# Kernel tuning notes

Measured on AMD Instinct MI355X. Metric: run time of the kernel, lower is better.

The kernel has to match this reference:

```python
import jax, jax.numpy as jnp
import numpy as np

S = 192          # seq_len = h*w = 24*8
FF = 2048        # dim_feedforward
CH = [171, 171, 170]  # d_model=512 chunked over 3 layers
EPS = 1e-5


def _bn(x, axes):
    # training-mode BatchNorm with gamma=1, beta=0 (default init; xavier only touches dim>1 weights)
    m = x.mean(axis=axes, keepdims=True)
    v = x.var(axis=axes, keepdims=True)
    return (x - m) / jnp.sqrt(v + EPS)


def _layer(tgt, mem, fc1_w, fc1_b, se, fc2_w, fc2_b, fc3_w, fc3_b):
    # tgt: [q, s, d], mem: [k, s, d]
    q, s, d = tgt.shape
    k = mem.shape[0]
    qy = tgt @ fc1_w.T + fc1_b            # [q, s, d]
    ky = mem @ fc1_w.T + fc1_b            # [k, s, d]
    # correlation volume gated by learned sigmoid bias -> [q, k, s, t]
    vol = jnp.einsum('qtd,ksd->qkst', qy, ky) * jax.nn.sigmoid(se)
    sc = jnp.concatenate([vol.max(axis=2).reshape(q * k, s),   # max over s -> per-t
                          vol.max(axis=3).reshape(q * k, s)],  # max over t -> per-s
                         axis=-1)                               # [q*k, 2s]
    sc = _bn(sc.reshape(-1, 1, s), (0, 2)).reshape(-1, s)       # bn1 over (N, L)
    sc = jax.nn.relu(_bn(sc @ fc2_w.T + fc2_b, (0,)))           # fc2 + bn2 + relu
    sc = sc @ fc3_w.T + fc3_b                                   # [2*q*k, 1]
    sc = _bn(sc.reshape(-1, 2).sum(-1, keepdims=True), (0,))    # combine halves + bn3
    return sc.reshape(q, k)


def _forward(gallery, query, params):
    # gallery/query: NCHW -> [B, H, W, C]; tgt = gallery (memory in TransMatcher), memory arg = query
    g = jnp.transpose(gallery, (0, 2, 3, 1))
    f = jnp.transpose(query, (0, 2, 3, 1))
    q, k = g.shape[0], f.shape[0]
    g = g.reshape(q, S, -1)
    f = f.reshape(k, S, -1)
    start = 0
    score = jnp.zeros((q, k), dtype=g.dtype)
    for i, c in enumerate(CH):
        score = score + _layer(g[..., start:start + c], f[..., start:start + c], *params[i])
        start += c
    # decoder norm: BatchNorm1d(1) over flattened scores
    return _bn(score.reshape(-1, 1), (0,)).reshape(q, k)


def setup_inputs() -> dict:
    key = jax.random.key(0)
    ks = iter(jax.random.split(key, 32))
    d = {
        'gallery': jax.random.normal(next(ks), (32, 512, 24, 8), jnp.float32),
        'query': jax.random.normal(next(ks), (32, 512, 24, 8), jnp.float32),
    }
    def xavier(k, shape):
        fan_in, fan_out = shape[1], shape[0]
        lim = np.sqrt(6.0 / (fan_in + fan_out)).astype(np.float32)
        return jax.random.uniform(k, shape, jnp.float32, -lim, lim)
    for i, c in enumerate(CH):
        d[f'l{i}_fc1_w'] = xavier(next(ks), (c, c))
        d[f'l{i}_fc1_b'] = jax.random.normal(next(ks), (c,), jnp.float32) * 0.02
        d[f'l{i}_se'] = xavier(next(ks), (S, S))
        d[f'l{i}_fc2_w'] = xavier(next(ks), (FF, S))
        d[f'l{i}_fc2_b'] = jax.random.normal(next(ks), (FF,), jnp.float32) * 0.02
        d[f'l{i}_fc3_w'] = xavier(next(ks), (1, FF))
        d[f'l{i}_fc3_b'] = jax.random.normal(next(ks), (1,), jnp.float32) * 0.02
    return d


def reference(gallery, query,
              l0_fc1_w, l0_fc1_b, l0_se, l0_fc2_w, l0_fc2_b, l0_fc3_w, l0_fc3_b,
              l1_fc1_w, l1_fc1_b, l1_se, l1_fc2_w, l1_fc2_b, l1_fc3_w, l1_fc3_b,
              l2_fc1_w, l2_fc1_b, l2_se, l2_fc2_w, l2_fc2_b, l2_fc3_w, l2_fc3_b):
    params = [
        (l0_fc1_w, l0_fc1_b, l0_se, l0_fc2_w, l0_fc2_b, l0_fc3_w, l0_fc3_b),
        (l1_fc1_w, l1_fc1_b, l1_se, l1_fc2_w, l1_fc2_b, l1_fc3_w, l1_fc3_b),
        (l2_fc1_w, l2_fc1_b, l2_se, l2_fc2_w, l2_fc2_b, l2_fc3_w, l2_fc3_b),
    ]
    return _forward(gallery, query, params)
```

## Files before the change

### kernel.cpp

```cpp
#include <hip/hip_runtime.h>
#include <math.h>

#define EPS 1e-5f
#define TOTAL_IN (32*512*192)
#define CPAD 176
#define KSTEPS 11
#define PACK_BK 6144

#define OFF_SIGSE 0u
#define OFF_W1T   110592u
#define OFF_QPACK 141568u
#define OFF_KPACK 1222912u
#define OFF_SC    2304256u
#define OFF_OUT2  2697472u
#define OFF_QSLAB OFF_OUT2
#define OFF_KSLAB (OFF_OUT2 + 1081344u)
#define OFF_COLP  6891776u
#define OFF_M2V2  7022848u
#define OFF_Y     7026944u
#define OFF_SCORE 7028992u

#define B_SIGSE 0u
#define B_W1T   110592u
#define B_SC    203520u
#define B_COLP  1383168u
#define B_M2R2  1579776u
#define B_Y     1592064u
#define B_SC3   1598208u
#define B_BIG   1601280u
#define B_SLAB  B_BIG
#define B_PACKF (B_BIG + 6488064u)
#define B_OUT2  B_BIG
#define B_TOTAL 14577408u

typedef __attribute__((ext_vector_type(8)))  short short8;
typedef __attribute__((ext_vector_type(16))) float f32x16;

__device__ __forceinline__ unsigned short f2bf(float x) {
    unsigned u = __float_as_uint(x);
    u += 0x7fffu + ((u >> 16) & 1u);
    return (unsigned short)(u >> 16);
}
__device__ __forceinline__ float bf2f(unsigned short h) {
    return __uint_as_float(((unsigned)h) << 16);
}

__device__ __forceinline__ void g2lds16(const void* g, void* l) {
    __builtin_amdgcn_global_load_lds((const __attribute__((address_space(1))) unsigned int*)g,
                                     (__attribute__((address_space(3))) unsigned int*)l, 16, 0, 0);
}

__global__ void k_sigse(const float* __restrict__ se0, const float* __restrict__ se1,
                        const float* __restrict__ se2, float* __restrict__ dst) {
    int idx = blockIdx.x * 256 + threadIdx.x;
    if (idx >= 3 * 36864) return;
    int l = idx / 36864, r = idx % 36864;
    const float* se = (l == 0) ? se0 : ((l == 1) ? se1 : se2);
    float x = se[r];
    dst[idx] = 1.0f / (1.0f + __expf(-x));
}


__global__ void k_w1t_b(const float* __restrict__ w1_0, const float* __restrict__ w1_1,
                        const float* __restrict__ w1_2, float* __restrict__ w1t) {
    int idx = blockIdx.x * 256 + threadIdx.x;
    if (idx >= 3 * CPAD * CPAD) return;
    int l = idx / (CPAD * CPAD), r = idx % (CPAD * CPAD);
    int i = r / CPAD, j = r % CPAD;
    int c = (l == 2) ? 170 : 171;
    const float* w1 = (l == 0) ? w1_0 : ((l == 1) ? w1_1 : w1_2);
    w1t[idx] = (i < c && j < c) ? w1[j * c + i] : 0.0f;
}

__global__ __launch_bounds__(256, 4)
void k_fc1_b(const float* __restrict__ g0, const float* __restrict__ g1,
             const float* __restrict__ w1tb,
             const float* __restrict__ b1_0, const float* __restrict__ b1_1,
             const float* __restrict__ b1_2, float* __restrict__ slabs) {
    __shared__ float As[2 * 16 * CPAD];
    __shared__ float Bs[2 * 16 * 64];
    const int quad = blockIdx.x, b = blockIdx.y, z = blockIdx.z;
    const int l = z >> 1, tensor = z & 1;
    const int c = (l == 2) ? 170 : 171, st = l * 171;
    const float* inp = tensor ? g1 : g0;
    const float* w1t = w1tb + (unsigned)l * (CPAD * CPAD);
    const float* b1 = (l == 0) ? b1_0 : ((l == 1) ? b1_1 : b1_2);
    float* dst = slabs + (size_t)z * 1081344u;
    const int tid = threadIdx.x, ty = tid >> 4, tx = tid & 15;
    const size_t boff = (size_t)b * 98304 + (size_t)st * 192 + (size_t)quad * 64;

    float acc[11][4];
#pragma unroll
    for (int i = 0; i < 11; ++i)
#pragma unroll
        for (int j = 0; j < 4; ++j) acc[i][j] = 0.0f;

    float4 v[4];
    auto load_chunk = [&](int ci) {
#pragma unroll
        for (int e = 0; e < 4; ++e) {
            int f = tid + (e << 8);
            if (f < 704) {
                v[e] = *(const float4*)(w1t + ci * 2816 + f * 4);
            } else if (f < 960) {
                int f2 = f - 704;
                int r = f2 >> 4, c4 = f2 & 15;
                size_t off = boff + (size_t)(ci * 16 + r) * 192 + c4 * 4;
                if (off > (size_t)(TOTAL_IN - 4)) off = (size_t)(TOTAL_IN - 4);
                v[e] = *(const float4*)(inp + off);
            }
        }
    };
    auto write_chunk = [&](int buf) {
        float* Ad = As + buf * 2816;
        float* Bd = Bs + buf * 1024;
#pragma unroll
        for (int e = 0; e < 4; ++e) {
            int f = tid + (e << 8);
            if (f < 704)      *(float4*)(Ad + f * 4) = v[e];
            else if (f < 960) *(float4*)(Bd + (f - 704) * 4) = v[e];
        }
    };

    load_chunk(0); write_chunk(0);
    __syncthreads();

    for (int ci = 0; ci < 11; ++ci) {
        const int buf = ci & 1;
        const bool pf = (ci + 1 < 11);
        if (pf) load_chunk(ci + 1);

        const float* Aw = As + buf * 2816 + ty * 11;
        const float* Bw = Bs + buf * 1024 + tx * 4;
#pragma unroll 2
        for (int kk = 0; kk < 16; ++kk) {
            float a[11];
#pragma unroll
            for (int i = 0; i < 11; ++i) a[i] = Aw[kk * CPAD + i];
            float4 B0 = *(const float4*)(Bw + kk * 64);
            float bb[4] = {B0.x, B0.y, B0.z, B0.w};
#pragma unroll
            for (int i = 0; i < 11; ++i)
#pragma unroll
                for (int j = 0; j < 4; ++j)
                    acc[i][j] = fmaf(a[i], bb[j], acc[i][j]);
        }
        if (pf) write_chunk(buf ^ 1);
        __syncthreads();
    }

    float* drow = dst + (size_t)b * (CPAD * 192) + quad * 64;
#pragma unroll
    for (int i = 0; i < 11; ++i) {
        int j = ty * 11 + i;
        bool valid = (j < c);
        float bias = valid ? b1[j] : 0.0f;
        float o[4];
#pragma unroll
        for (int jj = 0; jj < 4; ++jj) o[jj] = valid ? (acc[i][jj] + bias) : 0.0f;
        *(float4*)(drow + (size_t)j * 192 + tx * 4) = make_float4(o[0], o[1], o[2], o[3]);
    }
}

__global__ void k_pack_b(const float* __restrict__ slabs, short* __restrict__ packs) {
    const int kstep = blockIdx.x, b = blockIdx.y, z = blockIdx.z;
    const float* src = slabs + (size_t)z * 1081344u + (size_t)b * (CPAD * 192);
    short* dst = packs + (size_t)z * 2162688u + (size_t)(b * KSTEPS + kstep) * PACK_BK;
    const int t = threadIdx.x;
    const int tile = t >> 6, lane = t & 63;
    const int hf = (lane >> 5) & 1, col = lane & 31;
    const int dbase = kstep * 16 + hf * 8;
    const int x = tile * 32 + col;

    short8 H, L;
#pragma unroll
    for (int e = 0; e < 8; ++e) {
        float v = src[(size_t)(dbase + e) * 192 + x];
        unsigned short h = f2bf(v);
        unsigned short l = f2bf(v - bf2f(h));
        H[e] = (short)h;
        L[e] = (short)l;
    }
    ((short8*)dst)[(0 * 6 + tile) * 64 + lane] = H;
    ((short8*)dst)[(1 * 6 + tile) * 64 + lane] = L;
}

__global__ __launch_bounds__(256, 2)
void k_corr_b(const short* __restrict__ packs, const float* __restrict__ sigb,
              float* __restrict__ scb) {
    __shared__ short smem[2 * 12288];
    const int qk = blockIdx.x, l = blockIdx.y;
    const int q = qk >> 5, k = qk & 31;
    const int tid = threadIdx.x, lane = tid & 63, w = tid >> 6;
    const int ws = w >> 1, wt = w & 1;
    const short* qpack = packs + (size_t)(l * 2 + 0) * 2162688u;
    const short* kpack = packs + (size_t)(l * 2 + 1) * 2162688u;
    const float* sig = sigb + (unsigned)l * 36864u;
    float* sc = scb + (size_t)l * 393216u;
    const char* Abase = (const char*)(kpack + (size_t)k * KSTEPS * PACK_BK);
    const char* Bbase = (const char*)(qpack + (size_t)q * KSTEPS * PACK_BK);

    f32x16 acc[3][3];
#pragma unroll
    for (int i = 0; i < 3; ++i)
#pragma unroll
        for (int j = 0; j < 3; ++j)
#pragma unroll
            for (int r = 0; r < 16; ++r) acc[i][j][r] = 0.0f;

    auto stage = [&](int buf, int ks) {
#pragma unroll
        for (int u = 0; u < 6; ++u) {
            int c = u * 4 + w;
            const char* g = (c < 12 ? Abase + (size_t)ks * 12288 + c * 1024
                                    : Bbase + (size_t)ks * 12288 + (c - 12) * 1024) + lane * 16;
            g2lds16(g, (char*)smem + buf * 24576 + c * 1024);
        }
    };

    stage(0, 0);
    __syncthreads();

    int buf = 0;
    for (int ks = 0; ks < KSTEPS; ++ks) {
        if (ks + 1 < KSTEPS) stage(buf ^ 1, ks + 1);

        const short8* LA = (const short8*)((const char*)smem + buf * 24576);
        const short8* LB = (const short8*)((const char*)smem + buf * 24576 + 12288);
        short8 Ah[3], Al[3], Bh[3], Bl[3];
#pragma unroll
        for (int u = 0; u < 3; ++u) {
            Ah[u] = LA[(0 * 6 + ws * 3 + u) * 64 + lane];
            Al[u] = LA[(1 * 6 + ws * 3 + u) * 64 + lane];
            Bh[u] = LB[(0 * 6 + wt * 3 + u) * 64 + lane];
            Bl[u] = LB[(1 * 6 + wt * 3 + u) * 64 + lane];
        }
#pragma unroll
        for (int i = 0; i < 3; ++i)
#pragma unroll
            for (int j = 0; j < 3; ++j) {
                acc[i][j] = __builtin_amdgcn_mfma_f32_32x32x16_bf16(Ah[i], Bh[j], acc[i][j], 0, 0, 0);
                acc[i][j] = __builtin_amdgcn_mfma_f32_32x32x16_bf16(Al[i], Bh[j], acc[i][j], 0, 0, 0);
                acc[i][j] = __builtin_amdgcn_mfma_f32_32x32x16_bf16(Ah[i], Bl[j], acc[i][j], 0, 0, 0);
            }
        __syncthreads();
        buf ^= 1;
    }

    const int col = lane & 31, hf = lane >> 5;
    float* scr = (float*)smem;
    float cm[3] = {-3.0e38f, -3.0e38f, -3.0e38f};
#pragma unroll
    for (int i = 0; i < 3; ++i) {
        const int sbase = (ws * 3 + i) * 32;
        float rv[16];
#pragma unroll
        for (int r = 0; r < 16; ++r) rv[r] = -3.0e38f;
#pragma unroll
        for (int j = 0; j < 3; ++j) {
            const int tb = (wt * 3 + j) * 32 + col;
#pragma unroll
            for (int r = 0; r < 16; ++r) {
                int row = (r & 3) + 8 * (r >> 2) + 4 * hf;
                float v = acc[i][j][r] * sig[(size_t)(sbase + row) * 192 + tb];
                rv[r] = fmaxf(rv[r], v);
                cm[j] = fmaxf(cm[j], v);
            }
        }
#pragma unroll
        for (int m = 1; m < 32; m <<= 1)
#pragma unroll
            for (int r = 0; r < 16; ++r) rv[r] = fmaxf(rv[r], __shfl_xor(rv[r], m));
#pragma unroll
        for (int r = 0; r < 16; ++r)
            if (col == r)
                scr[384 + wt * 192 + sbase + (r & 3) + 8 * (r >> 2) + 4 * hf] = rv[r];
    }
#pragma unroll
    for (int j = 0; j < 3; ++j) {
        float c2 = fmaxf(cm[j], __shfl_xor(cm[j], 32));
        if (hf == 0) scr[ws * 192 + (wt * 3 + j) * 32 + col] = c2;
    }
    __syncthreads();
    if (tid < 192) {
        sc[(size_t)(2 * qk) * 192 + tid]     = fmaxf(scr[tid], scr[192 + tid]);
        sc[(size_t)(2 * qk + 1) * 192 + tid] = fmaxf(scr[384 + tid], scr[384 + 192 + tid]);
    }
}

__global__ __launch_bounds__(256, 2)
void k_fc2c_b(const float* __restrict__ scb,
              const float* __restrict__ w2_0, const float* __restrict__ w2_1,
              const float* __restrict__ w2_2,
              float* __restrict__ out2b, float* __restrict__ colpb) {
    __shared__ float Ast[32 * 132];
    __shared__ float Bst[32 * 132];
    const int bm = blockIdx.x & 15, bn = blockIdx.x >> 4, l = blockIdx.y;
    const float* sc = scb + (size_t)l * 393216u;
    const float* w2 = (l == 0) ? w2_0 : ((l == 1) ? w2_1 : w2_2);
    float* out2 = out2b + (size_t)l * 4194304u;
    float* colp = colpb + (size_t)l * 65536u;
    const int r0 = bm * 128, c0 = bn * 128;
    const int tid = threadIdx.x, ty = tid >> 4, tx = tid & 15;
    const int r = tid >> 1, half = (tid & 1) * 16;

    float acc[8][8];
#pragma unroll
    for (int i = 0; i < 8; ++i)
#pragma unroll
        for (int j = 0; j < 8; ++j) acc[i][j] = 0.0f;

    for (int t0 = 0; t0 < 192; t0 += 32) {
        float4 av[4], bv[4];
        const float4* ga = (const float4*)(sc + (size_t)(r0 + r) * 192 + t0 + half);
        const float4* gb = (const float4*)(w2 + (size_t)(c0 + r) * 192 + t0 + half);
#pragma unroll
        for (int e = 0; e < 4; ++e) { av[e] = ga[e]; bv[e] = gb[e]; }
        __syncthreads();
#pragma unroll
        for (int e = 0; e < 4; ++e) {
            int t = half + 4 * e;
            Ast[(t + 0) * 132 + r] = av[e].x;  Bst[(t + 0) * 132 + r] = bv[e].x;
            Ast[(t + 1) * 132 + r] = av[e].y;  Bst[(t + 1) * 132 + r] = bv[e].y;
            Ast[(t + 2) * 132 + r] = av[e].z;  Bst[(t + 2) * 132 + r] = bv[e].z;
            Ast[(t + 3) * 132 + r] = av[e].w;  Bst[(t + 3) * 132 + r] = bv[e].w;
        }
        __syncthreads();
#pragma unroll 4
        for (int kk = 0; kk < 32; ++kk) {
            const float4* ap = (const float4*)(Ast + kk * 132 + ty * 8);
            const float4* bp = (const float4*)(Bst + kk * 132 + tx * 8);
            float4 A0 = ap[0], A1 = ap[1];
            float4 B0 = bp[0], B1 = bp[1];
            float a[8] = {A0.x, A0.y, A0.z, A0.w, A1.x, A1.y, A1.z, A1.w};
            float b[8] = {B0.x, B0.y, B0.z, B0.w, B1.x, B1.y, B1.z, B1.w};
#pragma unroll
            for (int i = 0; i < 8; ++i)
#pragma unroll
                for (int j = 0; j < 8; ++j)
                    acc[i][j] = fmaf(a[i], b[j], acc[i][j]);
        }
    }
#pragma unroll
    for (int i = 0; i < 8; ++i) {
        float4* op = (float4*)(out2 + (size_t)(r0 + ty * 8 + i) * 2048 + c0 + tx * 8);
        op[0] = make_float4(acc[i][0], acc[i][1], acc[i][2], acc[i][3]);
        op[1] = make_float4(acc[i][4], acc[i][5], acc[i][6], acc[i][7]);
    }
    float cs_[8], cq_[8];
#pragma unroll
    for (int jj = 0; jj < 8; ++jj) {
        float s = 0.0f, q2 = 0.0f;
#pragma unroll
        for (int i = 0; i < 8; ++i) { float v = acc[i][jj]; s += v; q2 += v * v; }
        cs_[jj] = s; cq_[jj] = q2;
    }
    __syncthreads();
#pragma unroll
    for (int jj = 0; jj < 8; ++jj) {
        Ast[ty * 128 + tx * 8 + jj] = cs_[jj];
        Bst[ty * 128 + tx * 8 + jj] = cq_[jj];
    }
    __syncthreads();
    if (tid < 128) {
        float s = 0.0f, q2 = 0.0f;
#pragma unroll
        for (int wv = 0; wv < 16; ++wv) { s += Ast[wv * 128 + tid]; q2 += Bst[wv * 128 + tid]; }
        colp[((size_t)bm * 2048 + c0 + tid) * 2 + 0] = s;
        colp[((size_t)bm * 2048 + c0 + tid) * 2 + 1] = q2;
    }
}

__global__ void k_colf_b(const float* __restrict__ colpb, float* __restrict__ m2r2b) {
    const int idx = blockIdx.x * 256 + threadIdx.x;
    if (idx >= 3 * 2048) return;
    const int l = idx >> 11, j = idx & 2047;
    const float* colp = colpb + (size_t)l * 65536u;
    float s = 0.0f, s2 = 0.0f;
    for (int bm = 0; bm < 16; ++bm) {
        s  += colp[((size_t)bm * 2048 + j) * 2 + 0];
        s2 += colp[((size_t)bm * 2048 + j) * 2 + 1];
    }
    float m = s * (1.0f / 2048.0f);
    float var = s2 * (1.0f / 2048.0f) - m * m;
    m2r2b[(size_t)l * 4096 + j * 2 + 0] = m;
    m2r2b[(size_t)l * 4096 + j * 2 + 1] = rsqrtf(var + EPS);
}

__global__ void k_fc3_b(const float* __restrict__ out2b, const float* __restrict__ m2r2b,
                        const float* __restrict__ w3_0, const float* __restrict__ w3_1,
                        const float* __restrict__ w3_2, float* __restrict__ yb) {
    const int rr = blockIdx.x, l = blockIdx.y;
    const float* out2 = out2b + (size_t)l * 4194304u;
    const float* m2r2 = m2r2b + (size_t)l * 4096u;
    const float* w3 = (l == 0) ? w3_0 : ((l == 1) ? w3_1 : w3_2);
    const int tid = threadIdx.x;
    __shared__ float red[4];
    float s = 0.0f;
    for (int j = tid; j < 2048; j += 256) {
        float2 mr = ((const float2*)m2r2)[j];
        float vv = (out2[(size_t)rr * 2048 + j] - mr.x) * mr.y;
        vv = fmaxf(vv, 0.0f);
        s += vv * w3[j];
    }
#pragma unroll
    for (int off = 32; off; off >>= 1) s += __shfl_xor(s, off);
    if ((tid & 63) == 0) red[tid >> 6] = s;
    __syncthreads();
    if (tid == 0) yb[(size_t)l * 2048 + rr] = red[0] + red[1] + red[2] + red[3];
}

__global__ void k_bn3_b(const float* __restrict__ yb, float* __restrict__ sc3) {
    const int l = blockIdx.x, tid = threadIdx.x;
    const float* y = yb + (size_t)l * 2048u;
    __shared__ float rs[4], rs2[4];
    float p[4]; float s = 0.0f, s2 = 0.0f;
#pragma unroll
    for (int u = 0; u < 4; ++u) {
        int i = tid + (u << 8);
        float vv = y[2 * i] + y[2 * i + 1];
        p[u] = vv; s += vv; s2 += vv * vv;
    }
#pragma unroll
    for (int off = 32; off; off >>= 1) { s += __shfl_xor(s, off); s2 += __shfl_xor(s2, off); }
    if ((tid & 63) == 0) { rs[tid >> 6] = s; rs2[tid >> 6] = s2; }
    __syncthreads();
    float S = rs[0] + rs[1] + rs[2] + rs[3];
    float S2 = rs2[0] + rs2[1] + rs2[2] + rs2[3];
    float m = S * (1.0f / 1024.0f);
    float var = S2 * (1.0f / 1024.0f) - m * m;
    float rstd = rsqrtf(var + EPS);
#pragma unroll
    for (int u = 0; u < 4; ++u) {
        int i = tid + (u << 8);
        sc3[(size_t)l * 1024 + i] = (p[u] - m) * rstd;
    }
}

__global__ void k_final3(const float* __restrict__ sc3, float* __restrict__ out) {
    const int tid = threadIdx.x;
    __shared__ float rs[4], rs2[4];
    float p[4]; float s = 0.0f, s2 = 0.0f;
#pragma unroll
    for (int u = 0; u < 4; ++u) {
        int i = tid + (u << 8);
        float vv = sc3[i] + sc3[1024 + i] + sc3[2048 + i];
        p[u] = vv; s += vv; s2 += vv * vv;
    }
#pragma unroll
    for (int off = 32; off; off >>= 1) { s += __shfl_xor(s, off); s2 += __shfl_xor(s2, off); }
    if ((tid & 63) == 0) { rs[tid >> 6] = s; rs2[tid >> 6] = s2; }
    __syncthreads();
    float S = rs[0] + rs[1] + rs[2] + rs[3];
    float S2 = rs2[0] + rs2[1] + rs2[2] + rs2[3];
    float m = S * (1.0f / 1024.0f);
    float var = S2 * (1.0f / 1024.0f) - m * m;
    float rstd = rsqrtf(var + EPS);
#pragma unroll
    for (int u = 0; u < 4; ++u) {
        int i = tid + (u << 8);
        out[i] = (p[u] - m) * rstd;
    }
}


__global__ void k_w1t(const float* __restrict__ w1, int c, float* __restrict__ w1t) {
    int idx = blockIdx.x * 256 + threadIdx.x;
    if (idx >= CPAD * CPAD) return;
    int i = idx / CPAD, j = idx % CPAD;
    w1t[idx] = (i < c && j < c) ? w1[j * c + i] : 0.0f;
}

__global__ __launch_bounds__(256, 4)
void k_fc1(const float* __restrict__ g0, const float* __restrict__ g1,
           const float* __restrict__ w1t, const float* __restrict__ b1,
           int c, int st, float* __restrict__ d0, float* __restrict__ d1) {
    __shared__ float As[2 * 16 * CPAD];
    __shared__ float Bs[2 * 16 * 64];
    const int quad = blockIdx.x, b = blockIdx.y, tensor = blockIdx.z;
    const float* inp = tensor ? g1 : g0;
    float* dst = tensor ? d1 : d0;
    const int tid = threadIdx.x, ty = tid >> 4, tx = tid & 15;
    const size_t boff = (size_t)b * 98304 + (size_t)st * 192 + (size_t)quad * 64;

    float acc[11][4];
#pragma unroll
    for (int i = 0; i < 11; ++i)
#pragma unroll
        for (int j = 0; j < 4; ++j) acc[i][j] = 0.0f;

    float4 v[4];
    auto load_chunk = [&](int ci) {
#pragma unroll
        for (int e = 0; e < 4; ++e) {
            int f = tid + (e << 8);
            if (f < 704) {
                v[e] = *(const float4*)(w1t + ci * 2816 + f * 4);
            } else if (f < 960) {
                int f2 = f - 704;
                int r = f2 >> 4, c4 = f2 & 15;
                size_t off = boff + (size_t)(ci * 16 + r) * 192 + c4 * 4;
                if (off > (size_t)(TOTAL_IN - 4)) off = (size_t)(TOTAL_IN - 4);
                v[e] = *(const float4*)(inp + off);
            }
        }
    };
    auto write_chunk = [&](int buf) {
        float* Ad = As + buf * 2816;
        float* Bd = Bs + buf * 1024;
#pragma unroll
        for (int e = 0; e < 4; ++e) {
            int f = tid + (e << 8);
            if (f < 704)      *(float4*)(Ad + f * 4) = v[e];
            else if (f < 960) *(float4*)(Bd + (f - 704) * 4) = v[e];
        }
    };

    load_chunk(0); write_chunk(0);
    __syncthreads();

    for (int ci = 0; ci < 11; ++ci) {
        const int buf = ci & 1;
        const bool pf = (ci + 1 < 11);
        if (pf) load_chunk(ci + 1);

        const float* Aw = As + buf * 2816 + ty * 11;
        const float* Bw = Bs + buf * 1024 + tx * 4;
#pragma unroll 2
        for (int kk = 0; kk < 16; ++kk) {
            float a[11];
#pragma unroll
            for (int i = 0; i < 11; ++i) a[i] = Aw[kk * CPAD + i];
            float4 B0 = *(const float4*)(Bw + kk * 64);
            float bb[4] = {B0.x, B0.y, B0.z, B0.w};
#pragma unroll
            for (int i = 0; i < 11; ++i)
#pragma unroll
                for (int j = 0; j < 4; ++j)
                    acc[i][j] = fmaf(a[i], bb[j], acc[i][j]);
        }
        if (pf) write_chunk(buf ^ 1);
        __syncthreads();
    }

    float* drow = dst + (size_t)b * (CPAD * 192) + quad * 64;
#pragma unroll
    for (int i = 0; i < 11; ++i) {
        int j = ty * 11 + i;
        bool valid = (j < c);
        float bias = valid ? b1[j] : 0.0f;
        float o[4];
#pragma unroll
        for (int jj = 0; jj < 4; ++jj) o[jj] = valid ? (acc[i][jj] + bias) : 0.0f;
        *(float4*)(drow + (size_t)j * 192 + tx * 4) = make_float4(o[0], o[1], o[2], o[3]);
    }
}

__global__ void k_pack(const float* __restrict__ qslab, const float* __restrict__ kslab,
                       short* __restrict__ qpack, short* __restrict__ kpack) {
    const int kstep = blockIdx.x, b = blockIdx.y, tensor = blockIdx.z;
    const float* src = (tensor ? kslab : qslab) + (size_t)b * (CPAD * 192);
    short* dst = (tensor ? kpack : qpack) + (size_t)(b * KSTEPS + kstep) * PACK_BK;
    const int t = threadIdx.x;
    const int tile = t >> 6, lane = t & 63;
    const int hf = (lane >> 5) & 1, col = lane & 31;
    const int dbase = kstep * 16 + hf * 8;
    const int x = tile * 32 + col;

    short8 H, L;
#pragma unroll
    for (int e = 0; e < 8; ++e) {
        float v = src[(size_t)(dbase + e) * 192 + x];
        unsigned short h = f2bf(v);
        unsigned short l = f2bf(v - bf2f(h));
        H[e] = (short)h;
        L[e] = (short)l;
    }
    ((short8*)dst)[(0 * 6 + tile) * 64 + lane] = H;
    ((short8*)dst)[(1 * 6 + tile) * 64 + lane] = L;
}

__global__ __launch_bounds__(256, 2)
void k_corr(const short* __restrict__ qpack, const short* __restrict__ kpack,
            const float* __restrict__ sig, float* __restrict__ sc) {
    __shared__ short smem[2 * 12288];
    const int qk = blockIdx.x, q = qk >> 5, k = qk & 31;
    const int tid = threadIdx.x, lane = tid & 63, w = tid >> 6;
    const int ws = w >> 1, wt = w & 1;
    const char* Abase = (const char*)(kpack + (size_t)k * KSTEPS * PACK_BK);
    const char* Bbase = (const char*)(qpack + (size_t)q * KSTEPS * PACK_BK);

    f32x16 acc[3][3];
#pragma unroll
    for (int i = 0; i < 3; ++i)
#pragma unroll
        for (int j = 0; j < 3; ++j)
#pragma unroll
            for (int r = 0; r < 16; ++r) acc[i][j][r] = 0.0f;

    auto stage = [&](int buf, int ks) {
#pragma unroll
        for (int u = 0; u < 6; ++u) {
            int c = u * 4 + w;
            const char* g = (c < 12 ? Abase + (size_t)ks * 12288 + c * 1024
                                    : Bbase + (size_t)ks * 12288 + (c - 12) * 1024) + lane * 16;
            g2lds16(g, (char*)smem + buf * 24576 + c * 1024);
        }
    };

    stage(0, 0);
    __syncthreads();

    int buf = 0;
    for (int ks = 0; ks < KSTEPS; ++ks) {
        if (ks + 1 < KSTEPS) stage(buf ^ 1, ks + 1);

        const short8* LA = (const short8*)((const char*)smem + buf * 24576);
        const short8* LB = (const short8*)((const char*)smem + buf * 24576 + 12288);
        short8 Ah[3], Al[3], Bh[3], Bl[3];
#pragma unroll
        for (int u = 0; u < 3; ++u) {
            Ah[u] = LA[(0 * 6 + ws * 3 + u) * 64 + lane];
            Al[u] = LA[(1 * 6 + ws * 3 + u) * 64 + lane];
            Bh[u] = LB[(0 * 6 + wt * 3 + u) * 64 + lane];
            Bl[u] = LB[(1 * 6 + wt * 3 + u) * 64 + lane];
        }
#pragma unroll
        for (int i = 0; i < 3; ++i)
#pragma unroll
            for (int j = 0; j < 3; ++j) {
                acc[i][j] = __builtin_amdgcn_mfma_f32_32x32x16_bf16(Ah[i], Bh[j], acc[i][j], 0, 0, 0);
                acc[i][j] = __builtin_amdgcn_mfma_f32_32x32x16_bf16(Al[i], Bh[j], acc[i][j], 0, 0, 0);
                acc[i][j] = __builtin_amdgcn_mfma_f32_32x32x16_bf16(Ah[i], Bl[j], acc[i][j], 0, 0, 0);
            }
        __syncthreads();
        buf ^= 1;
    }

    const int col = lane & 31, hf = lane >> 5;
    float* scr = (float*)smem;
    float cm[3] = {-3.0e38f, -3.0e38f, -3.0e38f};
#pragma unroll
    for (int i = 0; i < 3; ++i) {
        const int sbase = (ws * 3 + i) * 32;
        float rv[16];
#pragma unroll
        for (int r = 0; r < 16; ++r) rv[r] = -3.0e38f;
#pragma unroll
        for (int j = 0; j < 3; ++j) {
            const int tb = (wt * 3 + j) * 32 + col;
#pragma unroll
            for (int r = 0; r < 16; ++r) {
                int row = (r & 3) + 8 * (r >> 2) + 4 * hf;
                float v = acc[i][j][r] * sig[(size_t)(sbase + row) * 192 + tb];
                rv[r] = fmaxf(rv[r], v);
                cm[j] = fmaxf(cm[j], v);
            }
        }
#pragma unroll
        for (int m = 1; m < 32; m <<= 1)
#pragma unroll
            for (int r = 0; r < 16; ++r) rv[r] = fmaxf(rv[r], __shfl_xor(rv[r], m));
#pragma unroll
        for (int r = 0; r < 16; ++r)
            if (col == r)
                scr[384 + wt * 192 + sbase + (r & 3) + 8 * (r >> 2) + 4 * hf] = rv[r];
    }
#pragma unroll
    for (int j = 0; j < 3; ++j) {
        float c2 = fmaxf(cm[j], __shfl_xor(cm[j], 32));
        if (hf == 0) scr[ws * 192 + (wt * 3 + j) * 32 + col] = c2;
    }
    __syncthreads();
    if (tid < 192) {
        sc[(size_t)(2 * qk) * 192 + tid]     = fmaxf(scr[tid], scr[192 + tid]);
        sc[(size_t)(2 * qk + 1) * 192 + tid] = fmaxf(scr[384 + tid], scr[384 + 192 + tid]);
    }
}

__global__ __launch_bounds__(256, 2)
void k_fc2(const float* __restrict__ sc, const float* __restrict__ w2, float* __restrict__ out2) {
    __shared__ float Ast[32 * 132];
    __shared__ float Bst[32 * 132];
    const int bm = blockIdx.x & 15, bn = blockIdx.x >> 4;
    const int r0 = bm * 128, c0 = bn * 128;
    const int tid = threadIdx.x, ty = tid >> 4, tx = tid & 15;
    const int r = tid >> 1, half = (tid & 1) * 16;

    float acc[8][8];
#pragma unroll
    for (int i = 0; i < 8; ++i)
#pragma unroll
        for (int j = 0; j < 8; ++j) acc[i][j] = 0.0f;

    for (int t0 = 0; t0 < 192; t0 += 32) {
        float4 av[4], bv[4];
        const float4* ga = (const float4*)(sc + (size_t)(r0 + r) * 192 + t0 + half);
        const float4* gb = (const float4*)(w2 + (size_t)(c0 + r) * 192 + t0 + half);
#pragma unroll
        for (int e = 0; e < 4; ++e) { av[e] = ga[e]; bv[e] = gb[e]; }
        __syncthreads();
#pragma unroll
        for (int e = 0; e < 4; ++e) {
            int t = half + 4 * e;
            Ast[(t + 0) * 132 + r] = av[e].x;  Bst[(t + 0) * 132 + r] = bv[e].x;
            Ast[(t + 1) * 132 + r] = av[e].y;  Bst[(t + 1) * 132 + r] = bv[e].y;
            Ast[(t + 2) * 132 + r] = av[e].z;  Bst[(t + 2) * 132 + r] = bv[e].z;
            Ast[(t + 3) * 132 + r] = av[e].w;  Bst[(t + 3) * 132 + r] = bv[e].w;
        }
        __syncthreads();
#pragma unroll 4
        for (int kk = 0; kk < 32; ++kk) {
            const float4* ap = (const float4*)(Ast + kk * 132 + ty * 8);
            const float4* bp = (const float4*)(Bst + kk * 132 + tx * 8);
            float4 A0 = ap[0], A1 = ap[1];
            float4 B0 = bp[0], B1 = bp[1];
            float a[8] = {A0.x, A0.y, A0.z, A0.w, A1.x, A1.y, A1.z, A1.w};
            float b[8] = {B0.x, B0.y, B0.z, B0.w, B1.x, B1.y, B1.z, B1.w};
#pragma unroll
            for (int i = 0; i < 8; ++i)
#pragma unroll
                for (int j = 0; j < 8; ++j)
                    acc[i][j] = fmaf(a[i], b[j], acc[i][j]);
        }
    }
#pragma unroll
    for (int i = 0; i < 8; ++i) {
        float4* op = (float4*)(out2 + (size_t)(r0 + ty * 8 + i) * 2048 + c0 + tx * 8);
        op[0] = make_float4(acc[i][0], acc[i][1], acc[i][2], acc[i][3]);
        op[1] = make_float4(acc[i][4], acc[i][5], acc[i][6], acc[i][7]);
    }
}

__global__ void k_colp(const float* __restrict__ out2, float* __restrict__ colp) {
    const int bc = blockIdx.x & 7, br = blockIdx.x >> 3;
    const int j = bc * 256 + threadIdx.x;
    float s = 0.0f, s2 = 0.0f;
    for (int rr = br * 64; rr < br * 64 + 64; ++rr) {
        float vv = out2[(size_t)rr * 2048 + j];
        s += vv; s2 += vv * vv;
    }
    colp[((size_t)br * 2048 + j) * 2 + 0] = s;
    colp[((size_t)br * 2048 + j) * 2 + 1] = s2;
}

__global__ void k_colf(const float* __restrict__ colp, float* __restrict__ m2r2) {
    const int j = blockIdx.x * 256 + threadIdx.x;
    if (j >= 2048) return;
    float s = 0.0f, s2 = 0.0f;
    for (int br = 0; br < 32; ++br) {
        s  += colp[((size_t)br * 2048 + j) * 2 + 0];
        s2 += colp[((size_t)br * 2048 + j) * 2 + 1];
    }
    float m = s * (1.0f / 2048.0f);
    float var = s2 * (1.0f / 2048.0f) - m * m;
    m2r2[j * 2 + 0] = m;
    m2r2[j * 2 + 1] = rsqrtf(var + EPS);
}

__global__ void k_fc3(const float* __restrict__ out2, const float* __restrict__ m2r2,
                      const float* __restrict__ w3, float* __restrict__ y) {
    const int rr = blockIdx.x;
    const int tid = threadIdx.x;
    __shared__ float red[4];
    float s = 0.0f;
    for (int j = tid; j < 2048; j += 256) {
        float2 mr = ((const float2*)m2r2)[j];
        float vv = (out2[(size_t)rr * 2048 + j] - mr.x) * mr.y;
        vv = fmaxf(vv, 0.0f);
        s += vv * w3[j];
    }
#pragma unroll
    for (int off = 32; off; off >>= 1) s += __shfl_xor(s, off);
    if ((tid & 63) == 0) red[tid >> 6] = s;
    __syncthreads();
    if (tid == 0) y[rr] = red[0] + red[1] + red[2] + red[3];
}

__global__ void k_bn3(const float* __restrict__ y, float* __restrict__ score, int first) {
    const int tid = threadIdx.x;
    __shared__ float rs[4], rs2[4];
    float p[4]; float s = 0.0f, s2 = 0.0f;
#pragma unroll
    for (int u = 0; u < 4; ++u) {
        int i = tid + (u << 8);
        float vv = y[2 * i] + y[2 * i + 1];
        p[u] = vv; s += vv; s2 += vv * vv;
    }
#pragma unroll
    for (int off = 32; off; off >>= 1) { s += __shfl_xor(s, off); s2 += __shfl_xor(s2, off); }
    if ((tid & 63) == 0) { rs[tid >> 6] = s; rs2[tid >> 6] = s2; }
    __syncthreads();
    float S = rs[0] + rs[1] + rs[2] + rs[3];
    float S2 = rs2[0] + rs2[1] + rs2[2] + rs2[3];
    float m = S * (1.0f / 1024.0f);
    float var = S2 * (1.0f / 1024.0f) - m * m;
    float rstd = rsqrtf(var + EPS);
#pragma unroll
    for (int u = 0; u < 4; ++u) {
        int i = tid + (u << 8);
        float vv = (p[u] - m) * rstd;
        score[i] = first ? vv : (score[i] + vv);
    }
}

__global__ void k_final(const float* __restrict__ score, float* __restrict__ out) {
    const int tid = threadIdx.x;
    __shared__ float rs[4], rs2[4];
    float p[4]; float s = 0.0f, s2 = 0.0f;
#pragma unroll
    for (int u = 0; u < 4; ++u) {
        int i = tid + (u << 8);
        float vv = score[i];
        p[u] = vv; s += vv; s2 += vv * vv;
    }
#pragma unroll
    for (int off = 32; off; off >>= 1) { s += __shfl_xor(s, off); s2 += __shfl_xor(s2, off); }
    if ((tid & 63) == 0) { rs[tid >> 6] = s; rs2[tid >> 6] = s2; }
    __syncthreads();
    float S = rs[0] + rs[1] + rs[2] + rs[3];
    float S2 = rs2[0] + rs2[1] + rs2[2] + rs2[3];
    float m = S * (1.0f / 1024.0f);
    float var = S2 * (1.0f / 1024.0f) - m * m;
    float rstd = rsqrtf(var + EPS);
#pragma unroll
    for (int u = 0; u < 4; ++u) {
        int i = tid + (u << 8);
        out[i] = (p[u] - m) * rstd;
    }
}

extern "C" void kernel_launch(void* const* d_in, const int* in_sizes, int n_in,
                              void* d_out, int out_size, void* d_ws, size_t ws_size,
                              hipStream_t stream) {
    const float* gallery = (const float*)d_in[0];
    const float* query   = (const float*)d_in[1];
    float* ws = (float*)d_ws;

    const bool batched = (ws_size >= (size_t)B_TOTAL * sizeof(float));

    if (batched) {
        k_sigse<<<(3 * 36864 + 255) / 256, 256, 0, stream>>>(
            (const float*)d_in[2 + 0 * 7 + 2], (const float*)d_in[2 + 1 * 7 + 2],
            (const float*)d_in[2 + 2 * 7 + 2], ws + B_SIGSE);
        k_w1t_b<<<(3 * CPAD * CPAD + 255) / 256, 256, 0, stream>>>(
            (const float*)d_in[2 + 0 * 7 + 0], (const float*)d_in[2 + 1 * 7 + 0],
            (const float*)d_in[2 + 2 * 7 + 0], ws + B_W1T);
        k_fc1_b<<<dim3(3, 32, 6), 256, 0, stream>>>(
            gallery, query, ws + B_W1T,
            (const float*)d_in[2 + 0 * 7 + 1], (const float*)d_in[2 + 1 * 7 + 1],
            (const float*)d_in[2 + 2 * 7 + 1], ws + B_SLAB);
        k_pack_b<<<dim3(KSTEPS, 32, 6), 384, 0, stream>>>(ws + B_SLAB, (short*)(ws + B_PACKF));
        k_corr_b<<<dim3(1024, 3), 256, 0, stream>>>((const short*)(ws + B_PACKF),
                                                    ws + B_SIGSE, ws + B_SC);
        k_fc2c_b<<<dim3(256, 3), 256, 0, stream>>>(
            ws + B_SC,
            (const float*)d_in[2 + 0 * 7 + 3], (const float*)d_in[2 + 1 * 7 + 3],
            (const float*)d_in[2 + 2 * 7 + 3], ws + B_OUT2, ws + B_COLP);
        k_colf_b<<<24, 256, 0, stream>>>(ws + B_COLP, ws + B_M2R2);
        k_fc3_b<<<dim3(2048, 3), 256, 0, stream>>>(
            ws + B_OUT2, ws + B_M2R2,
            (const float*)d_in[2 + 0 * 7 + 5], (const float*)d_in[2 + 1 * 7 + 5],
            (const float*)d_in[2 + 2 * 7 + 5], ws + B_Y);
        k_bn3_b<<<3, 256, 0, stream>>>(ws + B_Y, ws + B_SC3);
        k_final3<<<1, 256, 0, stream>>>(ws + B_SC3, (float*)d_out);
        return;
    }

    const int cs[3] = {171, 171, 170};
    const int st[3] = {0, 171, 342};

    short* qpack = (short*)(ws + OFF_QPACK);
    short* kpack = (short*)(ws + OFF_KPACK);

    k_sigse<<<(3 * 36864 + 255) / 256, 256, 0, stream>>>(
        (const float*)d_in[2 + 0 * 7 + 2], (const float*)d_in[2 + 1 * 7 + 2],
        (const float*)d_in[2 + 2 * 7 + 2], ws + OFF_SIGSE);

    for (int l = 0; l < 3; ++l) {
        const float* w1 = (const float*)d_in[2 + l * 7 + 0];
        const float* b1 = (const float*)d_in[2 + l * 7 + 1];
        const float* w2 = (const float*)d_in[2 + l * 7 + 3];
        const float* w3 = (const float*)d_in[2 + l * 7 + 5];

        k_w1t<<<(CPAD * CPAD + 255) / 256, 256, 0, stream>>>(w1, cs[l], ws + OFF_W1T);
        k_fc1<<<dim3(3, 32, 2), 256, 0, stream>>>(gallery, query, ws + OFF_W1T, b1,
                                                  cs[l], st[l], ws + OFF_QSLAB, ws + OFF_KSLAB);
        k_pack<<<dim3(KSTEPS, 32, 2), 384, 0, stream>>>(ws + OFF_QSLAB, ws + OFF_KSLAB,
                                                        qpack, kpack);
        k_corr<<<1024, 256, 0, stream>>>(qpack, kpack, ws + OFF_SIGSE + l * 36864, ws + OFF_SC);
        k_fc2<<<256, 256, 0, stream>>>(ws + OFF_SC, w2, ws + OFF_OUT2);
        k_colp<<<256, 256, 0, stream>>>(ws + OFF_OUT2, ws + OFF_COLP);
        k_colf<<<8, 256, 0, stream>>>(ws + OFF_COLP, ws + OFF_M2V2);
        k_fc3<<<2048, 256, 0, stream>>>(ws + OFF_OUT2, ws + OFF_M2V2, w3, ws + OFF_Y);
        k_bn3<<<1, 256, 0, stream>>>(ws + OFF_Y, ws + OFF_SCORE, l == 0 ? 1 : 0);
    }
    k_final<<<1, 256, 0, stream>>>(ws + OFF_SCORE, (float*)d_out);
}
```

Before: 389.0 us.

## Move fc2 GEMM onto bf16x3 MFMA with packed operands from corr kernel

Replaces the FP32 SIMT fc2 GEMM with a split-bf16 (hi/lo, three-product) MFMA kernel. The corr kernel now writes its pooled scores directly in the MFMA-packed hi/lo bf16 layout, and a new kernel pre-packs fc2 weights the same way. The fc1 kernel also pads its weight tile to 12 rows per thread so it can use float4 LDS loads. This targets the FP32 FMA cost of the 2048x2048x192 GEMMs, at the price of an extra packing launch, a larger workspace, and a small precision change from the bf16x3 approximation.

Measured after the change: 373.2 us. -4.1%, faster.

```diff
diff --git a/kernel.cpp b/kernel.cpp
--- a/kernel.cpp
+++ b/kernel.cpp
@@ -4,6 +4,7 @@
 #define EPS 1e-5f
 #define TOTAL_IN (32*512*192)
 #define CPAD 176
+#define MPAD 192
 #define KSTEPS 11
 #define PACK_BK 6144
 
@@ -22,16 +23,17 @@
 
 #define B_SIGSE 0u
 #define B_W1T   110592u
-#define B_SC    203520u
-#define B_COLP  1383168u
-#define B_M2R2  1579776u
-#define B_Y     1592064u
-#define B_SC3   1598208u
-#define B_BIG   1601280u
+#define B_SCPF  211968u
+#define B_W2PF  1391616u
+#define B_COLP  2571264u
+#define B_M2R2  2767872u
+#define B_Y     2780160u
+#define B_SC3   2786304u
+#define B_BIG   2789376u
 #define B_SLAB  B_BIG
 #define B_PACKF (B_BIG + 6488064u)
 #define B_OUT2  B_BIG
-#define B_TOTAL 14577408u
+#define B_TOTAL 15765504u
 
 typedef __attribute__((ext_vector_type(8)))  short short8;
 typedef __attribute__((ext_vector_type(16))) float f32x16;
@@ -64,9 +66,9 @@
 __global__ void k_w1t_b(const float* __restrict__ w1_0, const float* __restrict__ w1_1,
                         const float* __restrict__ w1_2, float* __restrict__ w1t) {
     int idx = blockIdx.x * 256 + threadIdx.x;
-    if (idx >= 3 * CPAD * CPAD) return;
-    int l = idx / (CPAD * CPAD), r = idx % (CPAD * CPAD);
-    int i = r / CPAD, j = r % CPAD;
+    if (idx >= 3 * CPAD * MPAD) return;
+    int l = idx / (CPAD * MPAD), r = idx % (CPAD * MPAD);
+    int i = r / MPAD, j = r % MPAD;
     int c = (l == 2) ? 170 : 171;
     const float* w1 = (l == 0) ? w1_0 : ((l == 1) ? w1_1 : w1_2);
     w1t[idx] = (i < c && j < c) ? w1[j * c + i] : 0.0f;
@@ -77,21 +79,21 @@
              const float* __restrict__ w1tb,
              const float* __restrict__ b1_0, const float* __restrict__ b1_1,
              const float* __restrict__ b1_2, float* __restrict__ slabs) {
-    __shared__ float As[2 * 16 * CPAD];
+    __shared__ float As[2 * 16 * MPAD];
     __shared__ float Bs[2 * 16 * 64];
     const int quad = blockIdx.x, b = blockIdx.y, z = blockIdx.z;
     const int l = z >> 1, tensor = z & 1;
     const int c = (l == 2) ? 170 : 171, st = l * 171;
     const float* inp = tensor ? g1 : g0;
-    const float* w1t = w1tb + (unsigned)l * (CPAD * CPAD);
+    const float* w1t = w1tb + (unsigned)l * (CPAD * MPAD);
     const float* b1 = (l == 0) ? b1_0 : ((l == 1) ? b1_1 : b1_2);
     float* dst = slabs + (size_t)z * 1081344u;
     const int tid = threadIdx.x, ty = tid >> 4, tx = tid & 15;
     const size_t boff = (size_t)b * 98304 + (size_t)st * 192 + (size_t)quad * 64;
 
-    float acc[11][4];
-#pragma unroll
-    for (int i = 0; i < 11; ++i)
+    float acc[12][4];
+#pragma unroll
+    for (int i = 0; i < 12; ++i)
 #pragma unroll
         for (int j = 0; j < 4; ++j) acc[i][j] = 0.0f;
 
@@ -100,10 +102,10 @@
 #pragma unroll
         for (int e = 0; e < 4; ++e) {
             int f = tid + (e << 8);
-            if (f < 704) {
-                v[e] = *(const float4*)(w1t + ci * 2816 + f * 4);
-            } else if (f < 960) {
-                int f2 = f - 704;
+            if (f < 768) {
+                v[e] = *(const float4*)(w1t + ci * 3072 + f * 4);
+            } else {
+                int f2 = f - 768;
                 int r = f2 >> 4, c4 = f2 & 15;
                 size_t off = boff + (size_t)(ci * 16 + r) * 192 + c4 * 4;
                 if (off > (size_t)(TOTAL_IN - 4)) off = (size_t)(TOTAL_IN - 4);
@@ -112,13 +114,13 @@
         }
     };
     auto write_chunk = [&](int buf) {
-        float* Ad = As + buf * 2816;
+        float* Ad = As + buf * 3072;
         float* Bd = Bs + buf * 1024;
 #pragma unroll
         for (int e = 0; e < 4; ++e) {
             int f = tid + (e << 8);
-            if (f < 704)      *(float4*)(Ad + f * 4) = v[e];
-            else if (f < 960) *(float4*)(Bd + (f - 704) * 4) = v[e];
+            if (f < 768) *(float4*)(Ad + f * 4) = v[e];
+            else         *(float4*)(Bd + (f - 768) * 4) = v[e];
         }
     };
 
@@ -130,17 +132,17 @@
         const bool pf = (ci + 1 < 11);
         if (pf) load_chunk(ci + 1);
 
-        const float* Aw = As + buf * 2816 + ty * 11;
+        const float* Aw = As + buf * 3072 + ty * 12;
         const float* Bw = Bs + buf * 1024 + tx * 4;
 #pragma unroll 2
         for (int kk = 0; kk < 16; ++kk) {
-            float a[11];
-#pragma unroll
-            for (int i = 0; i < 11; ++i) a[i] = Aw[kk * CPAD + i];
+            const float4* ap = (const float4*)(Aw + kk * MPAD);
+            float4 A0 = ap[0], A1 = ap[1], A2 = ap[2];
+            float a[12] = {A0.x, A0.y, A0.z, A0.w, A1.x, A1.y, A1.z, A1.w, A2.x, A2.y, A2.z, A2.w};
             float4 B0 = *(const float4*)(Bw + kk * 64);
             float bb[4] = {B0.x, B0.y, B0.z, B0.w};
 #pragma unroll
-            for (int i = 0; i < 11; ++i)
+            for (int i = 0; i < 12; ++i)
 #pragma unroll
                 for (int j = 0; j < 4; ++j)
                     acc[i][j] = fmaf(a[i], bb[j], acc[i][j]);
@@ -151,8 +153,9 @@
 
     float* drow = dst + (size_t)b * (CPAD * 192) + quad * 64;
 #pragma unroll
-    for (int i = 0; i < 11; ++i) {
-        int j = ty * 11 + i;
+    for (int i = 0; i < 12; ++i) {
+        int j = ty * 12 + i;
+        if (j >= CPAD) continue;
         bool valid = (j < c);
         float bias = valid ? b1[j] : 0.0f;
         float o[4];
@@ -185,9 +188,34 @@
     ((short8*)dst)[(1 * 6 + tile) * 64 + lane] = L;
 }
 
+__global__ void k_w2p(const float* __restrict__ w2_0, const float* __restrict__ w2_1,
+                      const float* __restrict__ w2_2, short* __restrict__ w2p) {
+    const int jt = blockIdx.x, l = blockIdx.y;
+    const float* w2 = (l == 0) ? w2_0 : ((l == 1) ? w2_1 : w2_2);
+    short* WP = w2p + (size_t)l * 786432u;
+    const int tid = threadIdx.x, lane = tid & 63, sub = tid >> 6;
+    const int j = jt * 32 + (lane & 31), hf = lane >> 5;
+#pragma unroll
+    for (int kk = 0; kk < 3; ++kk) {
+        int ks = sub * 3 + kk;
+        const float4* src = (const float4*)(w2 + (size_t)j * 192 + ks * 16 + hf * 8);
+        float4 a = src[0], b = src[1];
+        float v[8] = {a.x, a.y, a.z, a.w, b.x, b.y, b.z, b.w};
+        short8 H, L;
+#pragma unroll
+        for (int e = 0; e < 8; ++e) {
+            unsigned short h = f2bf(v[e]);
+            H[e] = (short)h;
+            L[e] = (short)f2bf(v[e] - bf2f(h));
+        }
+        ((short8*)WP)[((jt * 12 + ks) * 2 + 0) * 64 + lane] = H;
+        ((short8*)WP)[((jt * 12 + ks) * 2 + 1) * 64 + lane] = L;
+    }
+}
+
 __global__ __launch_bounds__(256, 2)
 void k_corr_b(const short* __restrict__ packs, const float* __restrict__ sigb,
-              float* __restrict__ scb) {
+              short* __restrict__ scp) {
     __shared__ short smem[2 * 12288];
     const int qk = blockIdx.x, l = blockIdx.y;
     const int q = qk >> 5, k = qk & 31;
@@ -196,7 +224,7 @@
     const short* qpack = packs + (size_t)(l * 2 + 0) * 2162688u;
     const short* kpack = packs + (size_t)(l * 2 + 1) * 2162688u;
     const float* sig = sigb + (unsigned)l * 36864u;
-    float* sc = scb + (size_t)l * 393216u;
+    short* scpl = scp + (size_t)l * 786432u;
     const char* Abase = (const char*)(kpack + (size_t)k * KSTEPS * PACK_BK);
     const char* Bbase = (const char*)(qpack + (size_t)q * KSTEPS * PACK_BK);
 
@@ -282,92 +310,116 @@
         if (hf == 0) scr[ws * 192 + (wt * 3 + j) * 32 + col] = c2;
     }
     __syncthreads();
-    if (tid < 192) {
-        sc[(size_t)(2 * qk) * 192 + tid]     = fmaxf(scr[tid], scr[192 + tid]);
-        sc[(size_t)(2 * qk + 1) * 192 + tid] = fmaxf(scr[384 + tid], scr[384 + 192 + tid]);
+    if (tid < 96) {
+        const int row = tid / 48, rem = tid % 48;
+        const int ks2 = rem >> 2, hf2 = (rem >> 1) & 1, pl = rem & 1;
+        const int r = 2 * qk + row;
+        const float* s0 = scr + row * 384;
+        short8 o;
+#pragma unroll
+        for (int e = 0; e < 8; ++e) {
+            int t = ks2 * 16 + hf2 * 8 + e;
+            float v = fmaxf(s0[t], s0[192 + t]);
+            unsigned short h = f2bf(v);
+            o[e] = pl ? (short)f2bf(v - bf2f(h)) : (short)h;
+        }
+        ((short8*)scpl)[(((r >> 5) * 12 + ks2) * 2 + pl) * 64 + (hf2 * 32 + (r & 31))] = o;
     }
 }
 
 __global__ __launch_bounds__(256, 2)
-void k_fc2c_b(const float* __restrict__ scb,
-              const float* __restrict__ w2_0, const float* __restrict__ w2_1,
-              const float* __restrict__ w2_2,
+void k_fc2m_b(const short* __restrict__ scp, const short* __restrict__ w2p,
               float* __restrict__ out2b, float* __restrict__ colpb) {
-    __shared__ float Ast[32 * 132];
-    __shared__ float Bst[32 * 132];
-    const int bm = blockIdx.x & 15, bn = blockIdx.x >> 4, l = blockIdx.y;
-    const float* sc = scb + (size_t)l * 393216u;
-    const float* w2 = (l == 0) ? w2_0 : ((l == 1) ? w2_1 : w2_2);
+    __shared__ short smem[2 * 8192];
+    const int rblk = blockIdx.x & 15, nblk = blockIdx.x >> 4, l = blockIdx.y;
     float* out2 = out2b + (size_t)l * 4194304u;
     float* colp = colpb + (size_t)l * 65536u;
-    const int r0 = bm * 128, c0 = bn * 128;
-    const int tid = threadIdx.x, ty = tid >> 4, tx = tid & 15;
-    const int r = tid >> 1, half = (tid & 1) * 16;
-
-    float acc[8][8];
-#pragma unroll
-    for (int i = 0; i < 8; ++i)
-#pragma unroll
-        for (int j = 0; j < 8; ++j) acc[i][j] = 0.0f;
-
-    for (int t0 = 0; t0 < 192; t0 += 32) {
-        float4 av[4], bv[4];
-        const float4* ga = (const float4*)(sc + (size_t)(r0 + r) * 192 + t0 + half);
-        const float4* gb = (const float4*)(w2 + (size_t)(c0 + r) * 192 + t0 + half);
-#pragma unroll
-        for (int e = 0; e < 4; ++e) { av[e] = ga[e]; bv[e] = gb[e]; }
+    const int tid = threadIdx.x, lane = tid & 63, w = tid >> 6;
+    const int wr = w >> 1, wc = w & 1;
+    const char* SPb = (const char*)(scp + (size_t)l * 786432u + (size_t)rblk * 4 * 12288u);
+    const char* WPb = (const char*)(w2p + (size_t)l * 786432u + (size_t)nblk * 4 * 12288u);
+
+    f32x16 acc[2][2];
+#pragma unroll
+    for (int i = 0; i < 2; ++i)
+#pragma unroll
+        for (int j = 0; j < 2; ++j)
+#pragma unroll
+            for (int r = 0; r < 16; ++r) acc[i][j][r] = 0.0f;
+
+    auto stage = [&](int buf, int ks) {
+#pragma unroll
+        for (int u = 0; u < 4; ++u) {
+            int c = u * 4 + w;
+            const char* g = (c < 8 ? SPb + (c >> 1) * 24576 + ks * 2048 + (c & 1) * 1024
+                                   : WPb + ((c - 8) >> 1) * 24576 + ks * 2048 + (c & 1) * 1024) + lane * 16;
+            g2lds16(g, (char*)smem + buf * 16384 + c * 1024);
+        }
+    };
+
+    stage(0, 0);
+    __syncthreads();
+
+    int buf = 0;
+    for (int ks = 0; ks < 12; ++ks) {
+        if (ks + 1 < 12) stage(buf ^ 1, ks + 1);
+
+        const char* base = (const char*)smem + buf * 16384;
+        short8 Ah[2], Al[2], Bh[2], Bl[2];
+#pragma unroll
+        for (int mt = 0; mt < 2; ++mt) {
+            Ah[mt] = *(const short8*)(base + ((wr * 2 + mt) * 2 + 0) * 1024 + lane * 16);
+            Al[mt] = *(const short8*)(base + ((wr * 2 + mt) * 2 + 1) * 1024 + lane * 16);
+        }
+#pragma unroll
+        for (int nt = 0; nt < 2; ++nt) {
+            Bh[nt] = *(const short8*)(base + 8192 + ((wc * 2 + nt) * 2 + 0) * 1024 + lane * 16);
+            Bl[nt] = *(const short8*)(base + 8192 + ((wc * 2 + nt) * 2 + 1) * 1024 + lane * 16);
+        }
+#pragma unroll
+        for (int mt = 0; mt < 2; ++mt)
+#pragma unroll
+            for (int nt = 0; nt < 2; ++nt) {
+                acc[mt][nt] = __builtin_amdgcn_mfma_f32_32x32x16_bf16(Ah[mt], Bh[nt], acc[mt][nt], 0, 0, 0);
+                acc[mt][nt] = __builtin_amdgcn_mfma_f32_32x32x16_bf16(Al[mt], Bh[nt], acc[mt][nt], 0, 0, 0);
+                acc[mt][nt] = __builtin_amdgcn_mfma_f32_32x32x16_bf16(Ah[mt], Bl[nt], acc[mt][nt], 0, 0, 0);
+            }
         __syncthreads();
-#pragma unroll
-        for (int e = 0; e < 4; ++e) {
-            int t = half + 4 * e;
-            Ast[(t + 0) * 132 + r] = av[e].x;  Bst[(t + 0) * 132 + r] = bv[e].x;
-            Ast[(t + 1) * 132 + r] = av[e].y;  Bst[(t + 1) * 132 + r] = bv[e].y;
-            Ast[(t + 2) * 132 + r] = av[e].z;  Bst[(t + 2) * 132 + r] = bv[e].z;
-            Ast[(t + 3) * 132 + r] = av[e].w;  Bst[(t + 3) * 132 + r] = bv[e].w;
-        }
-        __syncthreads();
-#pragma unroll 4
-        for (int kk = 0; kk < 32; ++kk) {
-            const float4* ap = (const float4*)(Ast + kk * 132 + ty * 8);
-            const float4* bp = (const float4*)(Bst + kk * 132 + tx * 8);
-            float4 A0 = ap[0], A1 = ap[1];
-            float4 B0 = bp[0], B1 = bp[1];
-            float a[8] = {A0.x, A0.y, A0.z, A0.w, A1.x, A1.y, A1.z, A1.w};
-            float b[8] = {B0.x, B0.y, B0.z, B0.w, B1.x, B1.y, B1.z, B1.w};
-#pragma unroll
-            for (int i = 0; i < 8; ++i)
-#pragma unroll
-                for (int j = 0; j < 8; ++j)
-                    acc[i][j] = fmaf(a[i], b[j], acc[i][j]);
-        }
-    }
-#pragma unroll
-    for (int i = 0; i < 8; ++i) {
-        float4* op = (float4*)(out2 + (size_t)(r0 + ty * 8 + i) * 2048 + c0 + tx * 8);
-        op[0] = make_float4(acc[i][0], acc[i][1], acc[i][2], acc[i][3]);
-        op[1] = make_float4(acc[i][4], acc[i][5], acc[i][6], acc[i][7]);
-    }
-    float cs_[8], cq_[8];
-#pragma unroll
-    for (int jj = 0; jj < 8; ++jj) {
+        buf ^= 1;
+    }
+
+    const int hf = lane >> 5, cl = lane & 31;
+#pragma unroll
+    for (int mt = 0; mt < 2; ++mt)
+#pragma unroll
+        for (int nt = 0; nt < 2; ++nt) {
+            const int c0 = nblk * 128 + (wc * 2 + nt) * 32 + cl;
+#pragma unroll
+            for (int r = 0; r < 16; ++r) {
+                int row = rblk * 128 + (wr * 2 + mt) * 32 + (r & 3) + 8 * (r >> 2) + 4 * hf;
+                out2[(size_t)row * 2048 + c0] = acc[mt][nt][r];
+            }
+        }
+    float* cs = (float*)smem;
+    float* cq = cs + 512;
+#pragma unroll
+    for (int nt = 0; nt < 2; ++nt) {
         float s = 0.0f, q2 = 0.0f;
 #pragma unroll
-        for (int i = 0; i < 8; ++i) { float v = acc[i][jj]; s += v; q2 += v * v; }
-        cs_[jj] = s; cq_[jj] = q2;
-    }
-    __syncthreads();
-#pragma unroll
-    for (int jj = 0; jj < 8; ++jj) {
-        Ast[ty * 128 + tx * 8 + jj] = cs_[jj];
-        Bst[ty * 128 + tx * 8 + jj] = cq_[jj];
+        for (int mt = 0; mt < 2; ++mt)
+#pragma unroll
+            for (int r = 0; r < 16; ++r) { float v = acc[mt][nt][r]; s += v; q2 += v * v; }
+        int ci = (wc * 2 + nt) * 32 + cl;
+        cs[ci * 4 + wr * 2 + hf] = s;
+        cq[ci * 4 + wr * 2 + hf] = q2;
     }
     __syncthreads();
     if (tid < 128) {
         float s = 0.0f, q2 = 0.0f;
 #pragma unroll
-        for (int wv = 0; wv < 16; ++wv) { s += Ast[wv * 128 + tid]; q2 += Bst[wv * 128 + tid]; }
-        colp[((size_t)bm * 2048 + c0 + tid) * 2 + 0] = s;
-        colp[((size_t)bm * 2048 + c0 + tid) * 2 + 1] = q2;
+        for (int u = 0; u < 4; ++u) { s += cs[tid * 4 + u]; q2 += cq[tid * 4 + u]; }
+        colp[((size_t)rblk * 2048 + nblk * 128 + tid) * 2 + 0] = s;
+        colp[((size_t)rblk * 2048 + nblk * 128 + tid) * 2 + 1] = q2;
     }
 }
 
@@ -840,10 +892,13 @@
     const bool batched = (ws_size >= (size_t)B_TOTAL * sizeof(float));
 
     if (batched) {
+        short* scp = (short*)(ws + B_SCPF);
+        short* w2p = (short*)(ws + B_W2PF);
+
         k_sigse<<<(3 * 36864 + 255) / 256, 256, 0, stream>>>(
             (const float*)d_in[2 + 0 * 7 + 2], (const float*)d_in[2 + 1 * 7 + 2],
             (const float*)d_in[2 + 2 * 7 + 2], ws + B_SIGSE);
-        k_w1t_b<<<(3 * CPAD * CPAD + 255) / 256, 256, 0, stream>>>(
+        k_w1t_b<<<(3 * CPAD * MPAD + 255) / 256, 256, 0, stream>>>(
             (const float*)d_in[2 + 0 * 7 + 0], (const float*)d_in[2 + 1 * 7 + 0],
             (const float*)d_in[2 + 2 * 7 + 0], ws + B_W1T);
         k_fc1_b<<<dim3(3, 32, 6), 256, 0, stream>>>(
@@ -851,12 +906,12 @@
             (const float*)d_in[2 + 0 * 7 + 1], (const float*)d_in[2 + 1 * 7 + 1],
             (const float*)d_in[2 + 2 * 7 + 1], ws + B_SLAB);
         k_pack_b<<<dim3(KSTEPS, 32, 6), 384, 0, stream>>>(ws + B_SLAB, (short*)(ws + B_PACKF));
+        k_w2p<<<dim3(64, 3), 256, 0, stream>>>(
+            (const float*)d_in[2 + 0 * 7 + 3], (const float*)d_in[2 + 1 * 7 + 3],
+            (const float*)d_in[2 + 2 * 7 + 3], w2p);
         k_corr_b<<<dim3(1024, 3), 256, 0, stream>>>((const short*)(ws + B_PACKF),
-                                                    ws + B_SIGSE, ws + B_SC);
-        k_fc2c_b<<<dim3(256, 3), 256, 0, stream>>>(
-            ws + B_SC,
-            (const float*)d_in[2 + 0 * 7 + 3], (const float*)d_in[2 + 1 * 7 + 3],
-            (const float*)d_in[2 + 2 * 7 + 3], ws + B_OUT2, ws + B_COLP);
+                                                    ws + B_SIGSE, scp);
+        k_fc2m_b<<<dim3(256, 3), 256, 0, stream>>>(scp, w2p, ws + B_OUT2, ws + B_COLP);
         k_colf_b<<<24, 256, 0, stream>>>(ws + B_COLP, ws + B_M2R2);
         k_fc3_b<<<dim3(2048, 3), 256, 0, stream>>>(
             ws + B_OUT2, ws + B_M2R2,
```
